# Kernel tuning notes

Measured on AMD Instinct MI355X. Metric: run time of the kernel, lower is better.

Reference implementation:

```python
import jax, jax.numpy as jnp
import numpy as np

B, T, C, H, W = 1, 8, 128, 64, 64
F = 64  # num_feat


def setup_inputs() -> dict:
    key = jax.random.key(0)
    ks = jax.random.split(key, 8)
    return {
        "input1": jax.random.normal(ks[0], (B, T, C, H, W), jnp.float32),
        "input2": jax.random.normal(ks[1], (B, T, C, H, W), jnp.float32),
        "W1": jax.random.normal(ks[2], (F, C), jnp.float32) * 0.05,
        "b1": jax.random.normal(ks[3], (F,), jnp.float32) * 0.05,
        "W2": jax.random.normal(ks[4], (F, C), jnp.float32) * 0.05,
        "b2": jax.random.normal(ks[5], (F,), jnp.float32) * 0.05,
        "W3": jax.random.normal(ks[6], (F, C), jnp.float32) * 0.05,
        "b3": jax.random.normal(ks[7], (F,), jnp.float32) * 0.05,
    }


def reference(input1, input2, W1, b1, W2, b2, W3, b3):
    # act == 0 (ReLU branch). Conv1d(kernel=1) == per-position linear projection.
    b, t, c, h, w = input1.shape
    n = h * w
    x1 = input1.reshape(b, t, c, n)  # matches transpose(1,2).reshape then frame slice
    x2 = input2.reshape(b, t, c, n)
    q = jnp.einsum('fc,btcn->btnf', W1, x1) + b1          # [B,T,N,F]
    k = jnp.einsum('fc,btcn->btnf', W2, x2) + b2          # [B,T,N,F]
    g = jnp.einsum('fc,btcn->btnf', W3, x1) + b3          # [B,T,N,F]
    scores = jax.nn.relu(jnp.einsum('btnf,btmf->btnm', q, k))  # [B,T,N,N]
    out = jnp.einsum('btnm,btmf->btnf', scores, g)        # [B,T,N,F]
    # view([B,H,W,F]).permute(0,3,1,2), stacked over T -> [B,T,F,H,W]
    return out.reshape(b, t, h, w, -1).transpose(0, 1, 4, 2, 3)
```

## Files before the change

kernel.cpp:

```cpp
#include <hip/hip_runtime.h>
#include <hip/hip_bf16.h>

constexpr int T = 8;
constexpr int C = 128;
constexpr int N = 4096;
constexpr int F = 64;

typedef __bf16 bf16x8 __attribute__((ext_vector_type(8)));
typedef __bf16 bf16x4 __attribute__((ext_vector_type(4)));
typedef float  f32x4  __attribute__((ext_vector_type(4)));

__global__ __launch_bounds__(256) void prep_w_kernel(
    const float* __restrict__ W1, const float* __restrict__ W2,
    const float* __restrict__ W3, __bf16* __restrict__ Wb)
{
    int i = blockIdx.x * 256 + threadIdx.x;
    int p = i >> 13, r = i & 8191;
    const float* W = (p == 0) ? W1 : (p == 1) ? W2 : W3;
    Wb[i] = (__bf16)W[r];
}

__global__ __launch_bounds__(256) void zero_out_kernel(float* __restrict__ out)
{
    int i = blockIdx.x * 256 + threadIdx.x;
    ((f32x4*)out)[i] = (f32x4){0.f, 0.f, 0.f, 0.f};
}

__global__ __launch_bounds__(256) void proj_kernel(
    const float* __restrict__ x1, const float* __restrict__ x2,
    const __bf16* __restrict__ Wb,
    const float* __restrict__ b1, const float* __restrict__ b2,
    const float* __restrict__ b3,
    __bf16* __restrict__ Qb, __bf16* __restrict__ Kb, __bf16* __restrict__ Gw)
{
    const int t  = blockIdx.x >> 6;
    const int nb = blockIdx.x & 63;
    const int n0 = nb * 64;

    constexpr int XS = 136;
    __shared__ __bf16 Xt1[64 * XS];
    __shared__ __bf16 Xt2[64 * XS];

    const int tid = threadIdx.x;
    const int ng  = tid & 15;
    const int cgi = tid >> 4;

#pragma unroll
    for (int pass = 0; pass < 2; ++pass) {
        const int c0 = cgi * 4 + pass * 64;
        const size_t base = ((size_t)t * C + c0) * (size_t)N + n0 + ng * 4;
        f32x4 v1[4], v2[4];
#pragma unroll
        for (int i = 0; i < 4; ++i) {
            v1[i] = *(const f32x4*)&x1[base + (size_t)i * N];
            v2[i] = *(const f32x4*)&x2[base + (size_t)i * N];
        }
#pragma unroll
        for (int j = 0; j < 4; ++j) {
            bf16x4 o1, o2;
#pragma unroll
            for (int i = 0; i < 4; ++i) {
                o1[i] = (__bf16)v1[i][j];
                o2[i] = (__bf16)v2[i][j];
            }
            *(bf16x4*)&Xt1[(ng * 4 + j) * XS + c0] = o1;
            *(bf16x4*)&Xt2[(ng * 4 + j) * XS + c0] = o2;
        }
    }
    __syncthreads();

    const int wave = tid >> 6, lane = tid & 63;
    const int quad = lane >> 4, l16 = lane & 15;

    bf16x8 a1[4], a2[4];
#pragma unroll
    for (int cc = 0; cc < 4; ++cc) {
        a1[cc] = *(const bf16x8*)&Xt1[(wave * 16 + l16) * XS + cc * 32 + quad * 8];
        a2[cc] = *(const bf16x8*)&Xt2[(wave * 16 + l16) * XS + cc * 32 + quad * 8];
    }

#pragma unroll
    for (int p = 0; p < 2; ++p) {
        const __bf16* W    = Wb + (size_t)p * F * C;
        const float*  bias = p ? b2 : b1;
        __bf16*       O    = p ? Kb : Qb;

        f32x4 acc[4];
#pragma unroll
        for (int ft = 0; ft < 4; ++ft) acc[ft] = (f32x4){0.f, 0.f, 0.f, 0.f};
#pragma unroll
        for (int cc = 0; cc < 4; ++cc) {
#pragma unroll
            for (int ft = 0; ft < 4; ++ft) {
                bf16x8 wf = *(const bf16x8*)&W[(ft * 16 + l16) * C + cc * 32 + quad * 8];
                bf16x8 xf = p ? a2[cc] : a1[cc];
                acc[ft] = __builtin_amdgcn_mfma_f32_16x16x32_bf16(wf, xf, acc[ft], 0, 0, 0);
            }
        }
        const int n = n0 + wave * 16 + l16;
#pragma unroll
        for (int ft = 0; ft < 4; ++ft) {
            const int f0 = ft * 16 + quad * 4;
            f32x4 bv = *(const f32x4*)&bias[f0];
            bf16x4 o;
#pragma unroll
            for (int r = 0; r < 4; ++r) o[r] = (__bf16)(acc[ft][r] + bv[r]);
            *(bf16x4*)&O[((size_t)t * N + n) * F + f0] = o;
        }
    }

    {
        const __bf16* W3b = Wb + (size_t)2 * F * C;
        f32x4 acc[4];
#pragma unroll
        for (int ft = 0; ft < 4; ++ft) acc[ft] = (f32x4){0.f, 0.f, 0.f, 0.f};
#pragma unroll
        for (int cc = 0; cc < 4; ++cc) {
#pragma unroll
            for (int ft = 0; ft < 4; ++ft) {
                bf16x8 wf = *(const bf16x8*)&W3b[(ft * 16 + l16) * C + cc * 32 + quad * 8];
                acc[ft] = __builtin_amdgcn_mfma_f32_16x16x32_bf16(a1[cc], wf, acc[ft], 0, 0, 0);
            }
        }
        const int nr0 = n0 + wave * 16 + quad * 4;
#pragma unroll
        for (int ft = 0; ft < 4; ++ft) {
            const int f = ft * 16 + l16;
            const float bv = b3[f];
            bf16x4 o;
#pragma unroll
            for (int r = 0; r < 4; ++r) o[r] = (__bf16)(acc[ft][r] + bv);
            *(bf16x4*)&Gw[((size_t)t * F + f) * (size_t)N + nr0] = o;
        }
    }
}

constexpr int KSPLIT = 4;

__global__ __launch_bounds__(256) void attn_kernel(
    const __bf16* __restrict__ Qb, const __bf16* __restrict__ Kb,
    const __bf16* __restrict__ Gw, float* __restrict__ out)
{
    const int ks = blockIdx.x & (KSPLIT - 1);
    const int qb = (blockIdx.x / KSPLIT) & 31;
    const int t  = blockIdx.x / (KSPLIT * 32);
    const int q0 = qb * 128;

    constexpr int KS = 72;
    __shared__ __bf16 Kt[64 * KS];
    __shared__ __bf16 Gt[64 * KS];
    __shared__ __bf16 Sb[128 * KS];

    const int tid = threadIdx.x, wave = tid >> 6, lane = tid & 63;
    const int quad = lane >> 4, l16 = lane & 15;

    bf16x8 qf[2][2];
#pragma unroll
    for (int qg = 0; qg < 2; ++qg) {
        const __bf16* qrow = &Qb[((size_t)t * N + q0 + wave * 32 + qg * 16 + l16) * F];
        qf[qg][0] = *(const bf16x8*)&qrow[quad * 8];
        qf[qg][1] = *(const bf16x8*)&qrow[32 + quad * 8];
    }

    f32x4 oacc[4][2];
#pragma unroll
    for (int ft = 0; ft < 4; ++ft)
#pragma unroll
        for (int qg = 0; qg < 2; ++qg) oacc[ft][qg] = (f32x4){0.f, 0.f, 0.f, 0.f};

    const int kb_lo = ks * (N / 64 / KSPLIT);
    const int kb_hi = kb_lo + (N / 64 / KSPLIT);

    const int r8a = tid >> 3,          c8a = (tid & 7) * 8;
    const int r8b = (tid + 256) >> 3,  c8b = c8a;

    bf16x8 kv0, kv1, gv0, gv1;
    {
        const int k0 = kb_lo * 64;
        kv0 = *(const bf16x8*)&Kb[((size_t)t * N + k0 + r8a) * F + c8a];
        kv1 = *(const bf16x8*)&Kb[((size_t)t * N + k0 + r8b) * F + c8b];
        gv0 = *(const bf16x8*)&Gw[((size_t)t * F + r8a) * (size_t)N + k0 + c8a];
        gv1 = *(const bf16x8*)&Gw[((size_t)t * F + r8b) * (size_t)N + k0 + c8b];
    }

    for (int kb = kb_lo; kb < kb_hi; ++kb) {
        __syncthreads();
        *(bf16x8*)&Kt[r8a * KS + c8a] = kv0;
        *(bf16x8*)&Kt[r8b * KS + c8b] = kv1;
        *(bf16x8*)&Gt[r8a * KS + c8a] = gv0;
        *(bf16x8*)&Gt[r8b * KS + c8b] = gv1;
        __syncthreads();

        if (kb + 1 < kb_hi) {
            const int k0 = (kb + 1) * 64;
            kv0 = *(const bf16x8*)&Kb[((size_t)t * N + k0 + r8a) * F + c8a];
            kv1 = *(const bf16x8*)&Kb[((size_t)t * N + k0 + r8b) * F + c8b];
            gv0 = *(const bf16x8*)&Gw[((size_t)t * F + r8a) * (size_t)N + k0 + c8a];
            gv1 = *(const bf16x8*)&Gw[((size_t)t * F + r8b) * (size_t)N + k0 + c8b];
        }

#pragma unroll
        for (int nt = 0; nt < 4; ++nt) {
            bf16x8 k0f = *(const bf16x8*)&Kt[(nt * 16 + l16) * KS + quad * 8];
            bf16x8 k1f = *(const bf16x8*)&Kt[(nt * 16 + l16) * KS + 32 + quad * 8];
#pragma unroll
            for (int qg = 0; qg < 2; ++qg) {
                f32x4 s = (f32x4){0.f, 0.f, 0.f, 0.f};
                s = __builtin_amdgcn_mfma_f32_16x16x32_bf16(k0f, qf[qg][0], s, 0, 0, 0);
                s = __builtin_amdgcn_mfma_f32_16x16x32_bf16(k1f, qf[qg][1], s, 0, 0, 0);
                bf16x4 sp;
#pragma unroll
                for (int r = 0; r < 4; ++r) sp[r] = (__bf16)fmaxf(s[r], 0.f);
                *(bf16x4*)&Sb[(wave * 32 + qg * 16 + l16) * KS + nt * 16 + quad * 4] = sp;
            }
        }

        bf16x8 sf[2][2];
#pragma unroll
        for (int qg = 0; qg < 2; ++qg) {
            const __bf16* srow = &Sb[(wave * 32 + qg * 16 + l16) * KS];
            sf[qg][0] = *(const bf16x8*)&srow[quad * 8];
            sf[qg][1] = *(const bf16x8*)&srow[32 + quad * 8];
        }
#pragma unroll
        for (int ft = 0; ft < 4; ++ft) {
            bf16x8 g0 = *(const bf16x8*)&Gt[(ft * 16 + l16) * KS + quad * 8];
            bf16x8 g1 = *(const bf16x8*)&Gt[(ft * 16 + l16) * KS + 32 + quad * 8];
#pragma unroll
            for (int qg = 0; qg < 2; ++qg) {
                oacc[ft][qg] = __builtin_amdgcn_mfma_f32_16x16x32_bf16(g0, sf[qg][0], oacc[ft][qg], 0, 0, 0);
                oacc[ft][qg] = __builtin_amdgcn_mfma_f32_16x16x32_bf16(g1, sf[qg][1], oacc[ft][qg], 0, 0, 0);
            }
        }
    }

#pragma unroll
    for (int ft = 0; ft < 4; ++ft)
#pragma unroll
        for (int qg = 0; qg < 2; ++qg)
#pragma unroll
            for (int r = 0; r < 4; ++r) {
                int f = ft * 16 + quad * 4 + r;
                int q = q0 + wave * 32 + qg * 16 + l16;
                unsafeAtomicAdd(&out[((size_t)t * F + f) * (size_t)N + q], oacc[ft][qg][r]);
            }
}

extern "C" void kernel_launch(void* const* d_in, const int* in_sizes, int n_in,
                              void* d_out, int out_size, void* d_ws, size_t ws_size,
                              hipStream_t stream) {
    const float* x1 = (const float*)d_in[0];
    const float* x2 = (const float*)d_in[1];
    const float* W1 = (const float*)d_in[2];
    const float* b1 = (const float*)d_in[3];
    const float* W2 = (const float*)d_in[4];
    const float* b2 = (const float*)d_in[5];
    const float* W3 = (const float*)d_in[6];
    const float* b3 = (const float*)d_in[7];
    float* out = (float*)d_out;

    __bf16* Qb = (__bf16*)d_ws;
    __bf16* Kb = Qb + (size_t)T * N * F;
    __bf16* Gw = Kb + (size_t)T * N * F;
    __bf16* Wb = Gw + (size_t)T * N * F;

    prep_w_kernel<<<dim3(3 * F * C / 256), dim3(256), 0, stream>>>(W1, W2, W3, Wb);
    proj_kernel<<<dim3(T * (N / 64)), dim3(256), 0, stream>>>(
        x1, x2, Wb, b1, b2, b3, Qb, Kb, Gw);
    zero_out_kernel<<<dim3(T * F * N / 4 / 256), dim3(256), 0, stream>>>(out);
    attn_kernel<<<dim3(T * 32 * KSPLIT), dim3(256), 0, stream>>>(Qb, Kb, Gw, out);
}
```

Measured before the change: 156.5 us.

## Use 32x32x16 MFMA with register-resident scores via permlane32 swap, merge setup kernels

The attention kernel moves from 16x16x32 MFMA tiles to 32x32x16 tiles. The ReLU'd score tile is repacked in registers with v_permlane32_swap so it can feed the second MFMA directly, which removes the shared-memory round trip through the Sb buffer. The weight-prep and output-zeroing kernels are merged into one launch to save a kernel launch. The cost is more dependence on correct lane-layout reasoning for the permlane shuffle, plus the inline asm that relies on the gfx950 instruction.

```diff
diff --git a/kernel.cpp b/kernel.cpp
--- a/kernel.cpp
+++ b/kernel.cpp
@@ -8,22 +8,22 @@
 
 typedef __bf16 bf16x8 __attribute__((ext_vector_type(8)));
 typedef __bf16 bf16x4 __attribute__((ext_vector_type(4)));
+typedef __bf16 bf16x2 __attribute__((ext_vector_type(2)));
 typedef float  f32x4  __attribute__((ext_vector_type(4)));
-
-__global__ __launch_bounds__(256) void prep_w_kernel(
+typedef float  f32x16 __attribute__((ext_vector_type(16)));
+
+__global__ __launch_bounds__(256) void setup_kernel(
     const float* __restrict__ W1, const float* __restrict__ W2,
-    const float* __restrict__ W3, __bf16* __restrict__ Wb)
-{
-    int i = blockIdx.x * 256 + threadIdx.x;
-    int p = i >> 13, r = i & 8191;
-    const float* W = (p == 0) ? W1 : (p == 1) ? W2 : W3;
-    Wb[i] = (__bf16)W[r];
-}
-
-__global__ __launch_bounds__(256) void zero_out_kernel(float* __restrict__ out)
+    const float* __restrict__ W3, __bf16* __restrict__ Wb,
+    float* __restrict__ out)
 {
     int i = blockIdx.x * 256 + threadIdx.x;
     ((f32x4*)out)[i] = (f32x4){0.f, 0.f, 0.f, 0.f};
+    if (i < 3 * F * C) {
+        int p = i >> 13, r = i & 8191;
+        const float* W = (p == 0) ? W1 : (p == 1) ? W2 : W3;
+        Wb[i] = (__bf16)W[r];
+    }
 }
 
 __global__ __launch_bounds__(256) void proj_kernel(
@@ -149,24 +149,23 @@
     constexpr int KS = 72;
     __shared__ __bf16 Kt[64 * KS];
     __shared__ __bf16 Gt[64 * KS];
-    __shared__ __bf16 Sb[128 * KS];
 
     const int tid = threadIdx.x, wave = tid >> 6, lane = tid & 63;
-    const int quad = lane >> 4, l16 = lane & 15;
-
-    bf16x8 qf[2][2];
-#pragma unroll
-    for (int qg = 0; qg < 2; ++qg) {
-        const __bf16* qrow = &Qb[((size_t)t * N + q0 + wave * 32 + qg * 16 + l16) * F];
-        qf[qg][0] = *(const bf16x8*)&qrow[quad * 8];
-        qf[qg][1] = *(const bf16x8*)&qrow[32 + quad * 8];
-    }
-
-    f32x4 oacc[4][2];
-#pragma unroll
-    for (int ft = 0; ft < 4; ++ft)
-#pragma unroll
-        for (int qg = 0; qg < 2; ++qg) oacc[ft][qg] = (f32x4){0.f, 0.f, 0.f, 0.f};
+    const int m32 = lane & 31, hi = lane >> 5;
+
+    bf16x8 qf[4];
+    {
+        const __bf16* qrow = &Qb[((size_t)t * N + q0 + wave * 32 + m32) * F + hi * 8];
+#pragma unroll
+        for (int fc = 0; fc < 4; ++fc)
+            qf[fc] = *(const bf16x8*)(qrow + fc * 16);
+    }
+
+    f32x16 oacc[2];
+#pragma unroll
+    for (int ft = 0; ft < 2; ++ft)
+#pragma unroll
+        for (int r = 0; r < 16; ++r) oacc[ft][r] = 0.f;
 
     const int kb_lo = ks * (N / 64 / KSPLIT);
     const int kb_hi = kb_lo + (N / 64 / KSPLIT);
@@ -199,51 +198,57 @@
             gv1 = *(const bf16x8*)&Gw[((size_t)t * F + r8b) * (size_t)N + k0 + c8b];
         }
 
-#pragma unroll
-        for (int nt = 0; nt < 4; ++nt) {
-            bf16x8 k0f = *(const bf16x8*)&Kt[(nt * 16 + l16) * KS + quad * 8];
-            bf16x8 k1f = *(const bf16x8*)&Kt[(nt * 16 + l16) * KS + 32 + quad * 8];
-#pragma unroll
-            for (int qg = 0; qg < 2; ++qg) {
-                f32x4 s = (f32x4){0.f, 0.f, 0.f, 0.f};
-                s = __builtin_amdgcn_mfma_f32_16x16x32_bf16(k0f, qf[qg][0], s, 0, 0, 0);
-                s = __builtin_amdgcn_mfma_f32_16x16x32_bf16(k1f, qf[qg][1], s, 0, 0, 0);
-                bf16x4 sp;
-#pragma unroll
-                for (int r = 0; r < 4; ++r) sp[r] = (__bf16)fmaxf(s[r], 0.f);
-                *(bf16x4*)&Sb[(wave * 32 + qg * 16 + l16) * KS + nt * 16 + quad * 4] = sp;
-            }
-        }
-
-        bf16x8 sf[2][2];
-#pragma unroll
-        for (int qg = 0; qg < 2; ++qg) {
-            const __bf16* srow = &Sb[(wave * 32 + qg * 16 + l16) * KS];
-            sf[qg][0] = *(const bf16x8*)&srow[quad * 8];
-            sf[qg][1] = *(const bf16x8*)&srow[32 + quad * 8];
-        }
-#pragma unroll
-        for (int ft = 0; ft < 4; ++ft) {
-            bf16x8 g0 = *(const bf16x8*)&Gt[(ft * 16 + l16) * KS + quad * 8];
-            bf16x8 g1 = *(const bf16x8*)&Gt[(ft * 16 + l16) * KS + 32 + quad * 8];
-#pragma unroll
-            for (int qg = 0; qg < 2; ++qg) {
-                oacc[ft][qg] = __builtin_amdgcn_mfma_f32_16x16x32_bf16(g0, sf[qg][0], oacc[ft][qg], 0, 0, 0);
-                oacc[ft][qg] = __builtin_amdgcn_mfma_f32_16x16x32_bf16(g1, sf[qg][1], oacc[ft][qg], 0, 0, 0);
-            }
-        }
-    }
-
-#pragma unroll
-    for (int ft = 0; ft < 4; ++ft)
-#pragma unroll
-        for (int qg = 0; qg < 2; ++qg)
-#pragma unroll
-            for (int r = 0; r < 4; ++r) {
-                int f = ft * 16 + quad * 4 + r;
-                int q = q0 + wave * 32 + qg * 16 + l16;
-                unsafeAtomicAdd(&out[((size_t)t * F + f) * (size_t)N + q], oacc[ft][qg][r]);
-            }
+        bf16x8 ps[4];
+#pragma unroll
+        for (int kt = 0; kt < 2; ++kt) {
+            f32x16 s;
+#pragma unroll
+            for (int r = 0; r < 16; ++r) s[r] = 0.f;
+#pragma unroll
+            for (int fc = 0; fc < 4; ++fc) {
+                bf16x8 kf = *(const bf16x8*)&Kt[(kt * 32 + m32) * KS + fc * 16 + hi * 8];
+                s = __builtin_amdgcn_mfma_f32_32x32x16_bf16(kf, qf[fc], s, 0, 0, 0);
+            }
+            unsigned P[8];
+#pragma unroll
+            for (int m = 0; m < 8; ++m) {
+                union { bf16x2 h; unsigned u; } pk;
+                pk.h[0] = (__bf16)fmaxf(s[2 * m], 0.f);
+                pk.h[1] = (__bf16)fmaxf(s[2 * m + 1], 0.f);
+                P[m] = pk.u;
+            }
+            asm("v_permlane32_swap_b32 %0, %1" : "+v"(P[0]), "+v"(P[2]));
+            asm("v_permlane32_swap_b32 %0, %1" : "+v"(P[1]), "+v"(P[3]));
+            asm("v_permlane32_swap_b32 %0, %1" : "+v"(P[4]), "+v"(P[6]));
+            asm("v_permlane32_swap_b32 %0, %1" : "+v"(P[5]), "+v"(P[7]));
+            union { unsigned u[4]; bf16x8 v; } lo, hiu;
+            lo.u[0]  = P[0]; lo.u[1]  = P[1]; lo.u[2]  = P[2]; lo.u[3]  = P[3];
+            hiu.u[0] = P[4]; hiu.u[1] = P[5]; hiu.u[2] = P[6]; hiu.u[3] = P[7];
+            ps[kt * 2]     = lo.v;
+            ps[kt * 2 + 1] = hiu.v;
+        }
+
+#pragma unroll
+        for (int ft = 0; ft < 2; ++ft)
+#pragma unroll
+            for (int kt = 0; kt < 2; ++kt)
+#pragma unroll
+                for (int kc = 0; kc < 2; ++kc) {
+                    bf16x8 gfr = *(const bf16x8*)&Gt[(ft * 32 + m32) * KS +
+                                                     kt * 32 + kc * 16 + hi * 8];
+                    oacc[ft] = __builtin_amdgcn_mfma_f32_32x32x16_bf16(
+                        gfr, ps[kt * 2 + kc], oacc[ft], 0, 0, 0);
+                }
+    }
+
+    const int q = q0 + wave * 32 + m32;
+#pragma unroll
+    for (int ft = 0; ft < 2; ++ft)
+#pragma unroll
+        for (int r = 0; r < 16; ++r) {
+            int f = ft * 32 + (r & 3) + 8 * (r >> 2) + 4 * hi;
+            unsafeAtomicAdd(&out[((size_t)t * F + f) * (size_t)N + q], oacc[ft][r]);
+        }
 }
 
 extern "C" void kernel_launch(void* const* d_in, const int* in_sizes, int n_in,
@@ -264,9 +269,9 @@
     __bf16* Gw = Kb + (size_t)T * N * F;
     __bf16* Wb = Gw + (size_t)T * N * F;
 
-    prep_w_kernel<<<dim3(3 * F * C / 256), dim3(256), 0, stream>>>(W1, W2, W3, Wb);
+    setup_kernel<<<dim3(T * F * N / 4 / 256), dim3(256), 0, stream>>>(
+        W1, W2, W3, Wb, out);
     proj_kernel<<<dim3(T * (N / 64)), dim3(256), 0, stream>>>(
         x1, x2, Wb, b1, b2, b3, Qb, Kb, Gw);
-    zero_out_kernel<<<dim3(T * F * N / 4 / 256), dim3(256), 0, stream>>>(out);
     attn_kernel<<<dim3(T * 32 * KSPLIT), dim3(256), 0, stream>>>(Qb, Kb, Gw, out);
 }
```

Result: faster. 151.9 us (-2.9%).
